# Optimization experiments

Measured on AMD Instinct MI355X. Metric: run time of the kernel, lower is better.

Reference implementation:

```python
import jax, jax.numpy as jnp
import numpy as np

N = 50000   # nodes
E = 800000  # edges
IN = 128    # input_channels
HID = 256   # hidden_channels
G = 64      # graphs
R = 3       # num_relations
META = 38
EPS = 1e-5


def _glorot(key, shape):
    fan_in, fan_out = shape[-2], shape[-1]
    lim = np.sqrt(6.0 / (fan_in + fan_out)).astype(np.float32)
    return jax.random.uniform(key, shape, jnp.float32, -lim, lim)


def setup_inputs() -> dict:
    key = jax.random.key(0)
    ks = iter(jax.random.split(key, 40))
    inp = {}
    inp["x"] = jax.random.normal(next(ks), (N, IN), jnp.float32)
    inp["edge_attr"] = jax.random.normal(next(ks), (E, 1), jnp.float32)  # unused by module
    inp["edge_index"] = jax.random.randint(next(ks), (2, E), 0, N)
    inp["edge_type"] = jax.random.randint(next(ks), (E,), 0, R)
    inp["MetaData"] = jax.random.normal(next(ks), (G, META), jnp.float32)
    inp["batch"] = jnp.sort(jax.random.randint(next(ks), (N,), 0, G))
    dims = [(IN, 100), (100, HID), (HID, HID), (HID, HID)]
    for l, (din, dout) in enumerate(dims):
        inp[f"W{l}"] = _glorot(next(ks), (R, din, dout))      # per-relation weights
        inp[f"R{l}"] = _glorot(next(ks), (din, dout))          # root weight
        inp[f"b{l}"] = jnp.zeros((dout,), jnp.float32)         # conv bias
        inp[f"g{l}"] = jnp.ones((dout,), jnp.float32)          # BN gamma
        inp[f"bb{l}"] = jnp.zeros((dout,), jnp.float32)        # BN beta
    inp["lin1_w"] = _glorot(next(ks), (HID + META, 100))
    inp["lin1_b"] = jnp.zeros((100,), jnp.float32)
    inp["lin2_w"] = _glorot(next(ks), (100, 1))
    inp["lin2_b"] = jnp.zeros((1,), jnp.float32)
    return inp


def reference(x, edge_attr, edge_index, edge_type, MetaData, batch,
              W0, R0, b0, g0, bb0, W1, R1, b1, g1, bb1,
              W2, R2, b2, g2, bb2, W3, R3, b3, g3, bb3,
              lin1_w, lin1_b, lin2_w, lin2_b):
    src, dst = edge_index[0], edge_index[1]
    seg = edge_type * N + dst  # combined (relation, dst) segment id
    ones_e = jnp.ones((E,), x.dtype)
    cnt = jax.ops.segment_sum(ones_e, seg, num_segments=R * N).reshape(R, N, 1)
    cnt = jnp.maximum(cnt, 1.0)

    def conv(h, W, Rw, b):
        # per-relation transform then gather-scatter mean aggregation (PyG RGCNConv, aggr='mean')
        H = jnp.einsum('ni,rio->rno', h, W)          # [R,N,out]
        msg = H[edge_type, src]                       # [E,out]
        agg = jax.ops.segment_sum(msg, seg, num_segments=R * N)
        agg = agg.reshape(R, N, -1) / cnt
        return agg.sum(0) + h @ Rw + b

    def bn(h, g, bb):  # training-mode BatchNorm1d over nodes
        mu = h.mean(0)
        var = h.var(0)
        return (h - mu) * jax.lax.rsqrt(var + EPS) * g + bb

    for W, Rw, b, g, bb in [(W0, R0, b0, g0, bb0), (W1, R1, b1, g1, bb1),
                            (W2, R2, b2, g2, bb2), (W3, R3, b3, g3, bb3)]:
        x = bn(conv(x, W, Rw, b), g, bb)

    # global_mean_pool
    sums = jax.ops.segment_sum(x, batch, num_segments=G)
    cnts = jax.ops.segment_sum(jnp.ones((N, 1), x.dtype), batch, num_segments=G)
    xg = sums / jnp.maximum(cnts, 1.0)

    h = jnp.concatenate([xg, MetaData], axis=1) @ lin1_w + lin1_b
    # dropout p=0.5 is identity in eval mode
    return h @ lin2_w + lin2_b
```

## Files before the change

kernel.cpp:

```cpp
#include <hip/hip_runtime.h>
#include <hip/hip_bf16.h>

#define NN 50000
#define EE 800000
#define GG 64
#define RR 3
#define METAD 38
#define NSEG (RR*NN)
#define EPSV 1e-5f

typedef __bf16 bf_t;
typedef __attribute__((ext_vector_type(8))) __bf16 bf16x8;
typedef __attribute__((ext_vector_type(4))) __bf16 bf16x4;
typedef __attribute__((ext_vector_type(2))) __bf16 bf16x2;
typedef __attribute__((ext_vector_type(4))) float f32x4;
typedef __attribute__((address_space(1))) void gas_t;
typedef __attribute__((address_space(3))) void las_t;

__device__ __forceinline__ float loadf(const void* p, size_t i, int flag){
  return flag ? ((const float*)p)[i] : (float)(((const bf_t*)p)[i]);
}

__global__ __launch_bounds__(256) void detect_kernel(const void* __restrict__ xraw,
                                                     int* __restrict__ flag){
  __shared__ int found;
  if (threadIdx.x == 0) found = 0;
  __syncthreads();
  const unsigned short* u = (const unsigned short*)xraw;
  for (int i = threadIdx.x; i < 65536; i += 256){
    int e = (u[i] >> 7) & 0xFF;
    if (e >= 0xF0) found = 1;
  }
  __syncthreads();
  if (threadIdx.x == 0) *flag = found;
}

struct CvtJobs {
  const void* src[17];
  float* dst[17];
  int n[17];
};

__global__ __launch_bounds__(256) void cvt_many(CvtJobs j, const int* __restrict__ flag){
  int job = blockIdx.y;
  int i = blockIdx.x*256 + threadIdx.x;
  if (i < j.n[job]) j.dst[job][i] = loadf(j.src[job], i, *flag);
}

__global__ __launch_bounds__(256) void pack_w(const void* __restrict__ W,
                                              const void* __restrict__ R,
                                              bf_t* __restrict__ out,
                                              int D, int O, int dplog,
                                              const int* __restrict__ flag){
  int id = blockIdx.x*256 + threadIdx.x;
  int DP4 = 1 << (dplog + 2);
  int o = id >> (dplog + 2);
  int k = id & (DP4 - 1);
  int r = k >> dplog;
  int i = k & ((1 << dplog) - 1);
  float v = 0.f;
  int fl = *flag;
  if (i < D && o < O){
    if (r < 3) v = loadf(W, ((size_t)r*D + i)*O + o, fl);
    else       v = loadf(R, (size_t)i*O + o, fl);
  }
  out[(size_t)o*DP4 + k] = (bf_t)v;
}

__global__ __launch_bounds__(256) void counti_kernel(const int* __restrict__ ei,
                                                     const int* __restrict__ et,
                                                     int* __restrict__ cnt){
  int e = blockIdx.x*256 + threadIdx.x;
  if (e < EE) atomicAdd(&cnt[et[e]*NN + ei[EE + e]], 1);
}

__global__ __launch_bounds__(256) void rcnt_kernel(const int* __restrict__ cnt,
                                                   float* __restrict__ rcnt){
  int i = blockIdx.x*256 + threadIdx.x;
  if (i < NSEG) rcnt[i] = 1.0f / (float)max(cnt[i], 1);
}

__global__ __launch_bounds__(256) void scan1_kernel(const int* __restrict__ cnt,
                                                    int* __restrict__ segoff,
                                                    int* __restrict__ bsums){
  __shared__ int sh[256];
  int i = blockIdx.x*256 + threadIdx.x;
  int v = (i < NSEG) ? cnt[i] : 0;
  sh[threadIdx.x] = v;
  __syncthreads();
  for (int off = 1; off < 256; off <<= 1){
    int t = 0;
    if (threadIdx.x >= off) t = sh[threadIdx.x - off];
    __syncthreads();
    if (threadIdx.x >= off) sh[threadIdx.x] += t;
    __syncthreads();
  }
  if (i < NSEG) segoff[i] = sh[threadIdx.x] - v;
  if (threadIdx.x == 255) bsums[blockIdx.x] = sh[255];
}

__global__ __launch_bounds__(256) void scan2_kernel(int* __restrict__ bsums, int nb){
  __shared__ int sh[256];
  __shared__ int carry;
  if (threadIdx.x == 0) carry = 0;
  __syncthreads();
  for (int base = 0; base < nb; base += 256){
    int i = base + threadIdx.x;
    int v = (i < nb) ? bsums[i] : 0;
    sh[threadIdx.x] = v;
    __syncthreads();
    for (int off = 1; off < 256; off <<= 1){
      int t = 0;
      if (threadIdx.x >= off) t = sh[threadIdx.x - off];
      __syncthreads();
      if (threadIdx.x >= off) sh[threadIdx.x] += t;
      __syncthreads();
    }
    if (i < nb) bsums[i] = sh[threadIdx.x] - v + carry;
    __syncthreads();
    if (threadIdx.x == 0) carry += sh[255];
    __syncthreads();
  }
}

__global__ __launch_bounds__(256) void scan3_kernel(int* __restrict__ segoff,
                                                    const int* __restrict__ bsums){
  int i = blockIdx.x*256 + threadIdx.x;
  if (i < NSEG) segoff[i] += bsums[blockIdx.x];
  if (i == 0) segoff[NSEG] = EE;
}

__global__ __launch_bounds__(256) void curinit_kernel(const int* __restrict__ segoff,
                                                      int* __restrict__ cursor){
  int i = blockIdx.x*256 + threadIdx.x;
  if (i < NSEG) cursor[i] = segoff[i];
}

__global__ __launch_bounds__(256) void place_kernel(const int* __restrict__ ei,
                                                    const int* __restrict__ et,
                                                    int* __restrict__ cursor,
                                                    int* __restrict__ srcs){
  int e = blockIdx.x*256 + threadIdx.x;
  if (e < EE){
    int seg = et[e]*NN + ei[EE + e];
    int pos = atomicAdd(&cursor[seg], 1);
    srcs[pos] = ei[e];
  }
}

__global__ __launch_bounds__(128) void cvt_x(const void* __restrict__ x,
                                             bf_t* __restrict__ Ab,
                                             const int* __restrict__ flag){
  int d = blockIdx.x, t = threadIdx.x;
  Ab[(size_t)d*512 + 384 + t] = (bf_t)loadf(x, (size_t)d*128 + t, *flag);
}

template<int DP>
__global__ __launch_bounds__(256) void aggregate_wave(const bf_t* __restrict__ Ab, int lda,
                                                      const int* __restrict__ segoff,
                                                      const int* __restrict__ srcs,
                                                      const float* __restrict__ rcnt,
                                                      const bf_t* __restrict__ zrow,
                                                      bf_t* __restrict__ out){
  int wid = (blockIdx.x*256 + threadIdx.x) >> 6;
  if (wid >= NSEG) return;
  wid = __builtin_amdgcn_readfirstlane(wid);
  int lane = threadIdx.x & 63;
  int r = wid / NN;
  int d = wid - r*NN;
  int s0 = segoff[wid], s1 = segoff[wid + 1];
  float rc = rcnt[wid];
  const bf_t* in = Ab + 3*DP;

  if (DP == 256){
    float a0=0.f, a1=0.f, a2=0.f, a3=0.f;
    const int off = lane*4;
    const bf_t* zp = zrow + off;
    int e = s0;
    for (; e + 4 <= s1; e += 4){
      int sA = srcs[e], sB = srcs[e+1], sC = srcs[e+2], sD = srcs[e+3];
      uint2 vA = *(const uint2*)(in + (size_t)sA*lda + off);
      uint2 vB = *(const uint2*)(in + (size_t)sB*lda + off);
      uint2 vC = *(const uint2*)(in + (size_t)sC*lda + off);
      uint2 vD = *(const uint2*)(in + (size_t)sD*lda + off);
      a0 += __uint_as_float(vA.x << 16); a1 += __uint_as_float(vA.x & 0xFFFF0000u);
      a2 += __uint_as_float(vA.y << 16); a3 += __uint_as_float(vA.y & 0xFFFF0000u);
      a0 += __uint_as_float(vB.x << 16); a1 += __uint_as_float(vB.x & 0xFFFF0000u);
      a2 += __uint_as_float(vB.y << 16); a3 += __uint_as_float(vB.y & 0xFFFF0000u);
      a0 += __uint_as_float(vC.x << 16); a1 += __uint_as_float(vC.x & 0xFFFF0000u);
      a2 += __uint_as_float(vC.y << 16); a3 += __uint_as_float(vC.y & 0xFFFF0000u);
      a0 += __uint_as_float(vD.x << 16); a1 += __uint_as_float(vD.x & 0xFFFF0000u);
      a2 += __uint_as_float(vD.y << 16); a3 += __uint_as_float(vD.y & 0xFFFF0000u);
    }
    if (e < s1){
      int sA = srcs[e];
      int sB = srcs[min(e+1, s1-1)];
      int sC = srcs[min(e+2, s1-1)];
      const uint2* pA = (const uint2*)(in + (size_t)sA*lda + off);
      const uint2* pB = (e+1 < s1) ? (const uint2*)(in + (size_t)sB*lda + off) : (const uint2*)zp;
      const uint2* pC = (e+2 < s1) ? (const uint2*)(in + (size_t)sC*lda + off) : (const uint2*)zp;
      uint2 vA = *pA, vB = *pB, vC = *pC;
      a0 += __uint_as_float(vA.x << 16); a1 += __uint_as_float(vA.x & 0xFFFF0000u);
      a2 += __uint_as_float(vA.y << 16); a3 += __uint_as_float(vA.y & 0xFFFF0000u);
      a0 += __uint_as_float(vB.x << 16); a1 += __uint_as_float(vB.x & 0xFFFF0000u);
      a2 += __uint_as_float(vB.y << 16); a3 += __uint_as_float(vB.y & 0xFFFF0000u);
      a0 += __uint_as_float(vC.x << 16); a1 += __uint_as_float(vC.x & 0xFFFF0000u);
      a2 += __uint_as_float(vC.y << 16); a3 += __uint_as_float(vC.y & 0xFFFF0000u);
    }
    bf16x4 o = {(bf_t)(a0*rc), (bf_t)(a1*rc), (bf_t)(a2*rc), (bf_t)(a3*rc)};
    *(bf16x4*)(out + (size_t)d*lda + r*DP + off) = o;
  } else {
    float a0=0.f, a1=0.f;
    const int off = lane*2;
    const bf_t* zp = zrow + off;
    int e = s0;
    for (; e + 4 <= s1; e += 4){
      int sA = srcs[e], sB = srcs[e+1], sC = srcs[e+2], sD = srcs[e+3];
      unsigned vA = *(const unsigned*)(in + (size_t)sA*lda + off);
      unsigned vB = *(const unsigned*)(in + (size_t)sB*lda + off);
      unsigned vC = *(const unsigned*)(in + (size_t)sC*lda + off);
      unsigned vD = *(const unsigned*)(in + (size_t)sD*lda + off);
      a0 += __uint_as_float(vA << 16); a1 += __uint_as_float(vA & 0xFFFF0000u);
      a0 += __uint_as_float(vB << 16); a1 += __uint_as_float(vB & 0xFFFF0000u);
      a0 += __uint_as_float(vC << 16); a1 += __uint_as_float(vC & 0xFFFF0000u);
      a0 += __uint_as_float(vD << 16); a1 += __uint_as_float(vD & 0xFFFF0000u);
    }
    if (e < s1){
      int sA = srcs[e];
      int sB = srcs[min(e+1, s1-1)];
      int sC = srcs[min(e+2, s1-1)];
      const unsigned* pA = (const unsigned*)(in + (size_t)sA*lda + off);
      const unsigned* pB = (e+1 < s1) ? (const unsigned*)(in + (size_t)sB*lda + off) : (const unsigned*)zp;
      const unsigned* pC = (e+2 < s1) ? (const unsigned*)(in + (size_t)sC*lda + off) : (const unsigned*)zp;
      unsigned vA = *pA, vB = *pB, vC = *pC;
      a0 += __uint_as_float(vA << 16); a1 += __uint_as_float(vA & 0xFFFF0000u);
      a0 += __uint_as_float(vB << 16); a1 += __uint_as_float(vB & 0xFFFF0000u);
      a0 += __uint_as_float(vC << 16); a1 += __uint_as_float(vC & 0xFFFF0000u);
    }
    bf16x2 o = {(bf_t)(a0*rc), (bf_t)(a1*rc)};
    *(bf16x2*)(out + (size_t)d*lda + r*DP + off) = o;
  }
}

#define ISSUE4W(B_, KO_)                                                                              \
  { uint4* _b = &lds4[B_][0];                                                                         \
    __builtin_amdgcn_global_load_lds((gas_t*)(Ar0 + (KO_)), (las_t*)(_b + wave*128 + lane), 16, 0, 0);\
    __builtin_amdgcn_global_load_lds((gas_t*)(Ar1 + (KO_)), (las_t*)(_b + wave*128 + 64 + lane), 16, 0, 0);\
    __builtin_amdgcn_global_load_lds((gas_t*)(Br0 + (KO_)), (las_t*)(_b + 512 + wave*128 + lane), 16, 0, 0);\
    __builtin_amdgcn_global_load_lds((gas_t*)(Br1 + (KO_)), (las_t*)(_b + 512 + wave*128 + 64 + lane), 16, 0, 0); }

template<int NT>
__global__ __launch_bounds__(256, 4) void gemm_mfma2(const bf_t* __restrict__ A, int lda, int K,
                                                     const bf_t* __restrict__ Bt,
                                                     const float* __restrict__ bias,
                                                     float* __restrict__ C, int ldc, int O,
                                                     float* __restrict__ sums){
  __shared__ uint4 lds4[2][1088];
  __shared__ float colsum[2*NT];
  float* stage = (float*)lds4;

  int tid = threadIdx.x;
  int lane = tid & 63;
  int wave = tid >> 6;
  int row0 = blockIdx.x*128;
  int col0 = blockIdx.y*NT;
  int mw = (wave & 1) << 6;
  int nw = (wave >> 1) << 6;
  int l15 = lane & 15, quad = lane >> 4;
  f32x4 acc[4][4] = {};

  int skc8 = ((lane & 3) ^ ((lane >> 3) & 3)) * 8;
  int sr0 = row0 + wave*32 + (lane >> 2);      if (sr0 >= NN) sr0 = NN - 1;
  int sr1 = row0 + wave*32 + 16 + (lane >> 2); if (sr1 >= NN) sr1 = NN - 1;
  const bf_t* Ar0 = A + (size_t)sr0*lda + skc8;
  const bf_t* Ar1 = A + (size_t)sr1*lda + skc8;
  const bf_t* Br0 = Bt + (size_t)(col0 + wave*32 + (lane >> 2))*K + skc8;
  const bf_t* Br1 = Bt + (size_t)(col0 + wave*32 + 16 + (lane >> 2))*K + skc8;

  int niter = K >> 5;
  ISSUE4W(0, 0)
  ISSUE4W(1, 32)

  int sx = (l15 >> 1) & 3;
  for (int i = 0; i < niter; ++i){
    if (i + 1 < niter) asm volatile("s_waitcnt vmcnt(4)" ::: "memory");
    else               asm volatile("s_waitcnt vmcnt(0)" ::: "memory");
    __builtin_amdgcn_s_barrier();
    asm volatile("" ::: "memory");
    __builtin_amdgcn_sched_barrier(0);

    const uint4* As4 = &lds4[i & 1][0];
    const uint4* Bs4 = As4 + 512;
    bf16x8 af[4], bfv[4];
    #pragma unroll
    for (int mi = 0; mi < 4; ++mi){
      int R = mw + mi*16 + l15;
      af[mi] = *(const bf16x8*)&As4[R*4 + (quad ^ sx)];
    }
    #pragma unroll
    for (int ni = 0; ni < 4; ++ni){
      int Rb = nw + ni*16 + l15;
      bfv[ni] = *(const bf16x8*)&Bs4[Rb*4 + (quad ^ sx)];
    }
    #pragma unroll
    for (int mi = 0; mi < 4; ++mi)
      #pragma unroll
      for (int ni = 0; ni < 4; ++ni)
        acc[mi][ni] = __builtin_amdgcn_mfma_f32_16x16x32_bf16(af[mi], bfv[ni], acc[mi][ni], 0, 0, 0);

    asm volatile("s_waitcnt lgkmcnt(0)" ::: "memory");
    __builtin_amdgcn_s_barrier();
    if (i + 2 < niter) ISSUE4W(i & 1, (i + 2) << 5)
  }

  __syncthreads();
  colsum[tid] = 0.f;
  float bzv[4];
  #pragma unroll
  for (int ni = 0; ni < 4; ++ni){
    int col = col0 + nw + ni*16 + l15;
    bzv[ni] = (col < O) ? bias[col] : 0.f;
  }
  __syncthreads();

  #pragma unroll
  for (int ni = 0; ni < 4; ++ni){
    int lcol = nw + ni*16 + l15;
    int col = col0 + lcol;
    if (col < O){
      float scol = 0.f, qcol = 0.f;
      #pragma unroll
      for (int mi = 0; mi < 4; ++mi){
        int rbase = row0 + mw + mi*16 + quad*4;
        #pragma unroll
        for (int j = 0; j < 4; ++j){
          if (rbase + j < NN){
            float v = acc[mi][ni][j] + bzv[ni];
            scol += v; qcol += v*v;
          }
        }
      }
      atomicAdd(&colsum[lcol], scol);
      atomicAdd(&colsum[NT + lcol], qcol);
    }
  }

  constexpr int STR = NT + 4;
  int rl0 = tid >> 5;
  int colg = (tid & 31)*4;
  #pragma unroll
  for (int c = 0; c < 2; ++c){
    __syncthreads();
    if ((wave & 1) == c){
      #pragma unroll
      for (int mi = 0; mi < 4; ++mi)
        #pragma unroll
        for (int ni = 0; ni < 4; ++ni)
          #pragma unroll
          for (int j = 0; j < 4; ++j)
            stage[(mi*16 + quad*4 + j)*STR + nw + ni*16 + l15] = acc[mi][ni][j] + bzv[ni];
    }
    __syncthreads();
    #pragma unroll
    for (int p = 0; p < 8; ++p){
      int rl = p*8 + rl0;
      int gr = row0 + c*64 + rl;
      if (gr < NN)
        *(float4*)&C[(size_t)gr*ldc + col0 + colg] = *(const float4*)&stage[rl*STR + colg];
    }
  }

  __syncthreads();
  for (int c = tid; c < NT; c += 256){
    int col = col0 + c;
    if (col < O){
      unsafeAtomicAdd(&sums[col], colsum[c]);
      unsafeAtomicAdd(&sums[256 + col], colsum[NT + c]);
    }
  }
}

__global__ __launch_bounds__(256) void bn_finalize(const float* __restrict__ sums,
                                                   const float* __restrict__ g,
                                                   const float* __restrict__ bb,
                                                   float* __restrict__ scale,
                                                   float* __restrict__ shift, int dout){
  int c = threadIdx.x;
  if (c < dout){
    float mu = sums[c] * (1.0f/NN);
    float var = sums[256 + c] * (1.0f/NN) - mu*mu;
    float rstd = rsqrtf(fmaxf(var, 0.f) + EPSV);
    float s = rstd * g[c];
    scale[c] = s;
    shift[c] = bb[c] - mu*s;
  }
}

template<int DPN>
__global__ __launch_bounds__(DPN) void bn_cvt(const float* __restrict__ C, int ldc, int O,
                                              const float* __restrict__ scale,
                                              const float* __restrict__ shift,
                                              bf_t* __restrict__ Ab, int ldan){
  int d = blockIdx.x, t = threadIdx.x;
  float v = 0.f;
  if (t < O) v = C[(size_t)d*ldc + t]*scale[t] + shift[t];
  Ab[(size_t)d*ldan + 3*DPN + t] = (bf_t)v;
}

__device__ __forceinline__ int lower_bound(const int* __restrict__ a, int v){
  int lo = 0, hi = NN;
  while (lo < hi){ int m = (lo+hi) >> 1; if (a[m] < v) lo = m+1; else hi = m; }
  return lo;
}

__global__ __launch_bounds__(256) void pool_kernel(const bf_t* __restrict__ H,
                                                   const int* __restrict__ batch,
                                                   float* __restrict__ pooled){
  int g = blockIdx.x, sl = blockIdx.y;
  int start = lower_bound(batch, g), end = lower_bound(batch, g+1);
  int len = end - start;
  float inv = 1.0f / (float)max(len, 1);
  int chunk = (len + 7) >> 3;
  int s0 = start + sl*chunk;
  int s1 = min(s0 + chunk, end);
  float s = 0.f;
  for (int n = s0; n < s1; ++n) s += (float)H[(size_t)n*1024 + threadIdx.x];
  if (s1 > s0) unsafeAtomicAdd(&pooled[g*256 + threadIdx.x], s * inv);
}

__global__ __launch_bounds__(128) void final_kernel(const float* __restrict__ pooled,
                                                    const float* __restrict__ meta,
                                                    const float* __restrict__ w1,
                                                    const float* __restrict__ b1,
                                                    const float* __restrict__ w2,
                                                    const float* __restrict__ b2,
                                                    void* __restrict__ out,
                                                    const int* __restrict__ flag){
  int g = blockIdx.x;
  __shared__ float h1[100];
  __shared__ float red[128];
  int t = threadIdx.x;
  if (t < 100){
    float acc = b1[t];
    for (int k = 0; k < 256; ++k) acc += pooled[g*256 + k] * w1[k*100 + t];
    for (int k = 0; k < METAD; ++k) acc += meta[g*METAD + k] * w1[(256+k)*100 + t];
    h1[t] = acc;
  }
  __syncthreads();
  red[t] = (t < 100) ? h1[t] * w2[t] : 0.f;
  __syncthreads();
  for (int s = 64; s > 0; s >>= 1){
    if (t < s) red[t] += red[t + s];
    __syncthreads();
  }
  if (t == 0){
    float v = red[0] + b2[0];
    if (*flag) ((float*)out)[g] = v;
    else       ((__hip_bfloat16*)out)[g] = __float2bfloat16(v);
  }
}

extern "C" void kernel_launch(void* const* d_in, const int* in_sizes, int n_in,
                              void* d_out, int out_size, void* d_ws, size_t ws_size,
                              hipStream_t stream){
  const void* x    = d_in[0];
  const int*  ei   = (const int*)d_in[2];
  const int*  et   = (const int*)d_in[3];
  const int*  batch= (const int*)d_in[5];

  float* ws     = (float*)d_ws;
  int*   flag   = (int*)ws;
  float* rcnt   = ws + 16;
  int*   cnt    = (int*)(ws + 150016);
  int*   segoff = (int*)(ws + 300032);
  int*   bsums  = (int*)(ws + 450048);
  int*   srcs   = (int*)(ws + 451072);
  float* sums   = ws + 1251072;
  float* scale  = ws + 1251584;
  float* shift  = ws + 1251840;
  float* pooled = ws + 1252096;
  float* bc     = ws + 1268480;
  float* gc_    = ws + 1269348;
  float* bbc    = ws + 1270216;
  float* metaf  = ws + 1271084;
  float* w1f    = ws + 1273516;
  float* b1f    = ws + 1302916;
  float* w2f    = ws + 1303016;
  float* b2f_   = ws + 1303116;
  bf_t*  wt     = (bf_t*)(ws + 1303168);
  int*   cursor = (int*)(ws + 1663616);
  float* C      = ws + 1813632;
  bf_t*  Ab     = (bf_t*)(ws + 14613632);

  const size_t wtoff[4] = {0, 65536, 196608, 458752};

  detect_kernel<<<1, 256, 0, stream>>>(x, flag);

  const int vsz[4]  = {100, 256, 256, 256};
  const int voff[4] = {0, 100, 356, 612};
  float *bfp[4], *gf[4], *bbf[4];
  CvtJobs J;
  int nj = 0;
  for (int l = 0; l < 4; ++l){
    bfp[l] = bc + voff[l]; gf[l] = gc_ + voff[l]; bbf[l] = bbc + voff[l];
    J.src[nj] = d_in[6 + l*5 + 2]; J.dst[nj] = bfp[l]; J.n[nj] = vsz[l]; nj++;
    J.src[nj] = d_in[6 + l*5 + 3]; J.dst[nj] = gf[l];  J.n[nj] = vsz[l]; nj++;
    J.src[nj] = d_in[6 + l*5 + 4]; J.dst[nj] = bbf[l]; J.n[nj] = vsz[l]; nj++;
  }
  J.src[nj] = d_in[4];  J.dst[nj] = metaf; J.n[nj] = GG*METAD; nj++;
  J.src[nj] = d_in[26]; J.dst[nj] = w1f;   J.n[nj] = 29400; nj++;
  J.src[nj] = d_in[27]; J.dst[nj] = b1f;   J.n[nj] = 100; nj++;
  J.src[nj] = d_in[28]; J.dst[nj] = w2f;   J.n[nj] = 100; nj++;
  J.src[nj] = d_in[29]; J.dst[nj] = b2f_;  J.n[nj] = 1; nj++;
  cvt_many<<<dim3(115, nj), 256, 0, stream>>>(J, flag);

  const int din[4] = {128, 100, 256, 256};
  const int dou[4] = {100, 256, 256, 256};
  const int DP[4]  = {128, 128, 256, 256};
  const int dplog[4] = {7, 7, 8, 8};
  const int Op[4]  = {128, 256, 256, 256};
  for (int l = 0; l < 4; ++l){
    int total = Op[l] << (dplog[l] + 2);
    pack_w<<<total/256, 256, 0, stream>>>(d_in[6 + l*5 + 0], d_in[6 + l*5 + 1],
                                          wt + wtoff[l], din[l], dou[l], dplog[l], flag);
  }

  hipMemsetAsync(cnt, 0, NSEG*sizeof(int), stream);
  counti_kernel<<<(EE+255)/256, 256, 0, stream>>>(ei, et, cnt);
  rcnt_kernel<<<(NSEG+255)/256, 256, 0, stream>>>(cnt, rcnt);
  int nb = (NSEG + 255)/256;
  scan1_kernel<<<nb, 256, 0, stream>>>(cnt, segoff, bsums);
  scan2_kernel<<<1, 256, 0, stream>>>(bsums, nb);
  scan3_kernel<<<nb, 256, 0, stream>>>(segoff, bsums);
  curinit_kernel<<<nb, 256, 0, stream>>>(segoff, cursor);
  place_kernel<<<(EE+255)/256, 256, 0, stream>>>(ei, et, cursor, srcs);
  hipMemsetAsync(bsums, 0, 1024, stream);
  const bf_t* zrow = (const bf_t*)bsums;

  cvt_x<<<NN, 128, 0, stream>>>(x, Ab, flag);

  const int lda[4] = {512, 512, 1024, 1024};
  int aggBlocks = (NSEG + 3)/4;
  for (int l = 0; l < 4; ++l){
    int O = dou[l];
    if (DP[l] == 128)
      aggregate_wave<128><<<aggBlocks, 256, 0, stream>>>(Ab, lda[l], segoff, srcs, rcnt, zrow, Ab);
    else
      aggregate_wave<256><<<aggBlocks, 256, 0, stream>>>(Ab, lda[l], segoff, srcs, rcnt, zrow, Ab);

    hipMemsetAsync(sums, 0, 512*sizeof(float), stream);
    dim3 g2(391, Op[l]/128);
    gemm_mfma2<128><<<g2, 256, 0, stream>>>(Ab, lda[l], 4*DP[l], wt + wtoff[l], bfp[l],
                                            C, Op[l], O, sums);

    bn_finalize<<<1, 256, 0, stream>>>(sums, gf[l], bbf[l], scale, shift, O);

    int DPN = (l < 3) ? DP[l+1] : 256;
    int ldan = (l < 3) ? lda[l+1] : 1024;
    if (DPN == 128)
      bn_cvt<128><<<NN, 128, 0, stream>>>(C, Op[l], O, scale, shift, Ab, ldan);
    else
      bn_cvt<256><<<NN, 256, 0, stream>>>(C, Op[l], O, scale, shift, Ab, ldan);
  }

  hipMemsetAsync(pooled, 0, (size_t)GG*256*sizeof(float), stream);
  pool_kernel<<<dim3(GG, 8), 256, 0, stream>>>(Ab + 768, batch, pooled);
  final_kernel<<<GG, 128, 0, stream>>>(pooled, metaf, w1f, b1f, w2f, b2f_, d_out, flag);
}
```

Baseline: 861.5 us.

## Enlarge GEMM tile to 256x256 with 1024 threads and store bf16 output

The GEMM block grows from 128x128 with 256 threads to a 256-row by 256-column tile with 16 waves, so one block covers every output column and A is loaded once per row block. The intermediate C buffer changes from fp32 to bf16, and bn_cvt reads bf16, which halves write and read traffic between GEMM and BatchNorm. In exchange the grid shrinks to 196 blocks, fewer than the CU count, and BN is now applied to rounded values. The first layer, with only 128 padded columns, also computes and loads a wasted half tile of B rows.

```diff
diff --git a/kernel.cpp b/kernel.cpp
--- a/kernel.cpp
+++ b/kernel.cpp
@@ -242,64 +242,58 @@
   }
 }
 
-#define ISSUE4W(B_, KO_)                                                                              \
-  { uint4* _b = &lds4[B_][0];                                                                         \
-    __builtin_amdgcn_global_load_lds((gas_t*)(Ar0 + (KO_)), (las_t*)(_b + wave*128 + lane), 16, 0, 0);\
-    __builtin_amdgcn_global_load_lds((gas_t*)(Ar1 + (KO_)), (las_t*)(_b + wave*128 + 64 + lane), 16, 0, 0);\
-    __builtin_amdgcn_global_load_lds((gas_t*)(Br0 + (KO_)), (las_t*)(_b + 512 + wave*128 + lane), 16, 0, 0);\
-    __builtin_amdgcn_global_load_lds((gas_t*)(Br1 + (KO_)), (las_t*)(_b + 512 + wave*128 + 64 + lane), 16, 0, 0); }
+#define ISSUE2(B_, KO_)                                                                             \
+  { uint4* _b = &lds4[B_][0];                                                                       \
+    __builtin_amdgcn_global_load_lds((gas_t*)(ArG + (KO_)), (las_t*)(_b + wave*64), 16, 0, 0);      \
+    __builtin_amdgcn_global_load_lds((gas_t*)(BrG + (KO_)), (las_t*)(_b + 1024 + wave*64), 16, 0, 0); }
 
 template<int NT>
-__global__ __launch_bounds__(256, 4) void gemm_mfma2(const bf_t* __restrict__ A, int lda, int K,
-                                                     const bf_t* __restrict__ Bt,
-                                                     const float* __restrict__ bias,
-                                                     float* __restrict__ C, int ldc, int O,
-                                                     float* __restrict__ sums){
-  __shared__ uint4 lds4[2][1088];
+__global__ __launch_bounds__(1024, 4) void gemm_mfma2(const bf_t* __restrict__ A, int lda, int K,
+                                                      const bf_t* __restrict__ Bt,
+                                                      const float* __restrict__ bias,
+                                                      bf_t* __restrict__ C, int ldc, int O,
+                                                      float* __restrict__ sums){
+  __shared__ uint4 lds4[2][2048];
   __shared__ float colsum[2*NT];
   float* stage = (float*)lds4;
 
   int tid = threadIdx.x;
   int lane = tid & 63;
   int wave = tid >> 6;
-  int row0 = blockIdx.x*128;
-  int col0 = blockIdx.y*NT;
-  int mw = (wave & 1) << 6;
-  int nw = (wave >> 1) << 6;
+  int wr = wave & 3, wc = wave >> 2;
+  int row0 = blockIdx.x*256;
+  int col0 = 0;
   int l15 = lane & 15, quad = lane >> 4;
   f32x4 acc[4][4] = {};
 
   int skc8 = ((lane & 3) ^ ((lane >> 3) & 3)) * 8;
-  int sr0 = row0 + wave*32 + (lane >> 2);      if (sr0 >= NN) sr0 = NN - 1;
-  int sr1 = row0 + wave*32 + 16 + (lane >> 2); if (sr1 >= NN) sr1 = NN - 1;
-  const bf_t* Ar0 = A + (size_t)sr0*lda + skc8;
-  const bf_t* Ar1 = A + (size_t)sr1*lda + skc8;
-  const bf_t* Br0 = Bt + (size_t)(col0 + wave*32 + (lane >> 2))*K + skc8;
-  const bf_t* Br1 = Bt + (size_t)(col0 + wave*32 + 16 + (lane >> 2))*K + skc8;
+  int arow = row0 + wave*16 + (lane >> 2); if (arow >= NN) arow = NN - 1;
+  const bf_t* ArG = A + (size_t)arow*lda + skc8;
+  const bf_t* BrG = Bt + (size_t)(col0 + wave*16 + (lane >> 2))*K + skc8;
 
   int niter = K >> 5;
-  ISSUE4W(0, 0)
-  ISSUE4W(1, 32)
+  ISSUE2(0, 0)
+  ISSUE2(1, 32)
 
   int sx = (l15 >> 1) & 3;
   for (int i = 0; i < niter; ++i){
-    if (i + 1 < niter) asm volatile("s_waitcnt vmcnt(4)" ::: "memory");
+    if (i + 1 < niter) asm volatile("s_waitcnt vmcnt(2)" ::: "memory");
     else               asm volatile("s_waitcnt vmcnt(0)" ::: "memory");
     __builtin_amdgcn_s_barrier();
     asm volatile("" ::: "memory");
     __builtin_amdgcn_sched_barrier(0);
 
     const uint4* As4 = &lds4[i & 1][0];
-    const uint4* Bs4 = As4 + 512;
+    const uint4* Bs4 = As4 + 1024;
     bf16x8 af[4], bfv[4];
     #pragma unroll
     for (int mi = 0; mi < 4; ++mi){
-      int R = mw + mi*16 + l15;
+      int R = wr*64 + mi*16 + l15;
       af[mi] = *(const bf16x8*)&As4[R*4 + (quad ^ sx)];
     }
     #pragma unroll
     for (int ni = 0; ni < 4; ++ni){
-      int Rb = nw + ni*16 + l15;
+      int Rb = wc*64 + ni*16 + l15;
       bfv[ni] = *(const bf16x8*)&Bs4[Rb*4 + (quad ^ sx)];
     }
     #pragma unroll
@@ -310,28 +304,28 @@
 
     asm volatile("s_waitcnt lgkmcnt(0)" ::: "memory");
     __builtin_amdgcn_s_barrier();
-    if (i + 2 < niter) ISSUE4W(i & 1, (i + 2) << 5)
-  }
-
-  __syncthreads();
-  colsum[tid] = 0.f;
+    if (i + 2 < niter) ISSUE2(i & 1, (i + 2) << 5)
+  }
+
+  __syncthreads();
+  if (tid < 2*NT) colsum[tid] = 0.f;
   float bzv[4];
   #pragma unroll
   for (int ni = 0; ni < 4; ++ni){
-    int col = col0 + nw + ni*16 + l15;
+    int col = col0 + wc*64 + ni*16 + l15;
     bzv[ni] = (col < O) ? bias[col] : 0.f;
   }
   __syncthreads();
 
   #pragma unroll
   for (int ni = 0; ni < 4; ++ni){
-    int lcol = nw + ni*16 + l15;
+    int lcol = wc*64 + ni*16 + l15;
     int col = col0 + lcol;
     if (col < O){
       float scol = 0.f, qcol = 0.f;
       #pragma unroll
       for (int mi = 0; mi < 4; ++mi){
-        int rbase = row0 + mw + mi*16 + quad*4;
+        int rbase = row0 + wr*64 + mi*16 + quad*4;
         #pragma unroll
         for (int j = 0; j < 4; ++j){
           if (rbase + j < NN){
@@ -347,31 +341,34 @@
 
   constexpr int STR = NT + 4;
   int rl0 = tid >> 5;
-  int colg = (tid & 31)*4;
+  int cg = (tid & 31)*8;
   #pragma unroll
-  for (int c = 0; c < 2; ++c){
-    __syncthreads();
-    if ((wave & 1) == c){
+  for (int c = 0; c < 8; ++c){
+    __syncthreads();
+    if (wr == (c >> 1)){
+      int base = (c & 1)*32;
       #pragma unroll
-      for (int mi = 0; mi < 4; ++mi)
+      for (int m2 = 0; m2 < 2; ++m2){
+        int mi = (c & 1)*2 + m2;
         #pragma unroll
         for (int ni = 0; ni < 4; ++ni)
           #pragma unroll
           for (int j = 0; j < 4; ++j)
-            stage[(mi*16 + quad*4 + j)*STR + nw + ni*16 + l15] = acc[mi][ni][j] + bzv[ni];
-    }
-    __syncthreads();
-    #pragma unroll
-    for (int p = 0; p < 8; ++p){
-      int rl = p*8 + rl0;
-      int gr = row0 + c*64 + rl;
-      if (gr < NN)
-        *(float4*)&C[(size_t)gr*ldc + col0 + colg] = *(const float4*)&stage[rl*STR + colg];
-    }
-  }
-
-  __syncthreads();
-  for (int c = tid; c < NT; c += 256){
+            stage[(mi*16 + quad*4 + j - base)*STR + wc*64 + ni*16 + l15] = acc[mi][ni][j] + bzv[ni];
+      }
+    }
+    __syncthreads();
+    int gr = row0 + c*32 + rl0;
+    if (gr < NN && cg < ldc){
+      const float* sp = &stage[rl0*STR + cg];
+      bf16x8 o = {(bf_t)sp[0], (bf_t)sp[1], (bf_t)sp[2], (bf_t)sp[3],
+                  (bf_t)sp[4], (bf_t)sp[5], (bf_t)sp[6], (bf_t)sp[7]};
+      *(bf16x8*)&C[(size_t)gr*ldc + col0 + cg] = o;
+    }
+  }
+
+  __syncthreads();
+  for (int c = tid; c < NT; c += 1024){
     int col = col0 + c;
     if (col < O){
       unsafeAtomicAdd(&sums[col], colsum[c]);
@@ -397,13 +394,13 @@
 }
 
 template<int DPN>
-__global__ __launch_bounds__(DPN) void bn_cvt(const float* __restrict__ C, int ldc, int O,
+__global__ __launch_bounds__(DPN) void bn_cvt(const bf_t* __restrict__ C, int ldc, int O,
                                               const float* __restrict__ scale,
                                               const float* __restrict__ shift,
                                               bf_t* __restrict__ Ab, int ldan){
   int d = blockIdx.x, t = threadIdx.x;
   float v = 0.f;
-  if (t < O) v = C[(size_t)d*ldc + t]*scale[t] + shift[t];
+  if (t < O) v = (float)C[(size_t)d*ldc + t]*scale[t] + shift[t];
   Ab[(size_t)d*ldan + 3*DPN + t] = (bf_t)v;
 }
 
@@ -489,7 +486,7 @@
   float* b2f_   = ws + 1303116;
   bf_t*  wt     = (bf_t*)(ws + 1303168);
   int*   cursor = (int*)(ws + 1663616);
-  float* C      = ws + 1813632;
+  bf_t*  C      = (bf_t*)(ws + 1813632);
   bf_t*  Ab     = (bf_t*)(ws + 14613632);
 
   const size_t wtoff[4] = {0, 65536, 196608, 458752};
@@ -549,9 +546,8 @@
       aggregate_wave<256><<<aggBlocks, 256, 0, stream>>>(Ab, lda[l], segoff, srcs, rcnt, zrow, Ab);
 
     hipMemsetAsync(sums, 0, 512*sizeof(float), stream);
-    dim3 g2(391, Op[l]/128);
-    gemm_mfma2<128><<<g2, 256, 0, stream>>>(Ab, lda[l], 4*DP[l], wt + wtoff[l], bfp[l],
-                                            C, Op[l], O, sums);
+    gemm_mfma2<256><<<dim3(196, 1), 1024, 0, stream>>>(Ab, lda[l], 4*DP[l], wt + wtoff[l], bfp[l],
+                                                       C, Op[l], O, sums);
 
     bn_finalize<<<1, 256, 0, stream>>>(sums, gf[l], bbf[l], scale, shift, O);
 
```

Result: no change. 845.8 us (-1.8%).
